# Performance work log

Measured on AMD Instinct MI355X. Metric: run time of the kernel, lower is better.

Reference implementation:

```python
import jax, jax.numpy as jnp
import numpy as np

K, N = 64, 4096

def setup_inputs() -> dict:
    key = jax.random.key(0)
    k1, k2 = jax.random.split(key)
    zs = jax.random.uniform(k1, (K, N), dtype=jnp.float32)        # K candidate schedules
    X = jax.random.uniform(k2, (N, N), dtype=jnp.float32)         # channel gain matrix
    var_noise = jnp.asarray(1.0, dtype=jnp.float32)
    return {"zs": zs, "X": X, "var_noise": var_noise}

def reference(zs, X, var_noise):
    # Original per-sample math: all_info[i,j] = z[j]*X[i,j]
    #   numerators   = diag(all_info) = z * diag(X)
    #   denominators = row_sum(all_info) - numerators = X @ z - numerators
    # Batched over K zs: one GEMM instead of K O(n^2) elementwise products.
    row_sums = jnp.einsum('kn,in->ki', zs, X)       # [K, N] = (X @ z_k)_i
    numerators = zs * jnp.diagonal(X)[None, :]      # [K, N]
    denominators = row_sums - numerators            # [K, N]
    per_sample = -jnp.sum(numerators / (var_noise + denominators), axis=1)  # [K]
    return jnp.sum(per_sample) / zs.shape[0]
```

## Files before the change

### kernel.cpp

```cpp
#include <hip/hip_runtime.h>

#define N_DIM 4096

typedef float f4  __attribute__((ext_vector_type(4)));
typedef short s8v __attribute__((ext_vector_type(8)));

#if defined(__has_builtin)
#if __has_builtin(__builtin_amdgcn_cvt_pk_bf16_f32)
#define HAVE_CVT_PK 1
#endif
#endif

static __device__ __forceinline__ unsigned int f2bf_pair(float lo, float hi) {
#ifdef HAVE_CVT_PK
    typedef __bf16 bf2 __attribute__((ext_vector_type(2)));
    bf2 p = __builtin_amdgcn_cvt_pk_bf16_f32(lo, hi);
    return __builtin_bit_cast(unsigned int, p);
#else
    unsigned int ul = __builtin_bit_cast(unsigned int, lo);
    unsigned int uh = __builtin_bit_cast(unsigned int, hi);
    ul = ul + 0x7fffu + ((ul >> 16) & 1u);
    uh = uh + 0x7fffu + ((uh >> 16) & 1u);
    return (uh & 0xffff0000u) | (ul >> 16);
#endif
}

static __device__ __forceinline__ s8v cvt8(f4 a, f4 b) {
    unsigned int u4[4] = { f2bf_pair(a[0], a[1]), f2bf_pair(a[2], a[3]),
                           f2bf_pair(b[0], b[1]), f2bf_pair(b[2], b[3]) };
    return __builtin_bit_cast(s8v, u4);
}

#define MFMA(a, b, c) __builtin_amdgcn_mfma_f32_16x16x32_bf16((a), (b), (c), 0, 0, 0)

__global__ void zero_out_kernel(float* __restrict__ out) {
    if (threadIdx.x == 0 && blockIdx.x == 0) out[0] = 0.f;
}

__global__ __launch_bounds__(256) void gemm_part_kernel(
    const float* __restrict__ zs, const float* __restrict__ X,
    float* __restrict__ part) {
    __shared__ s8v zsP[2][512];
    __shared__ s8v xP [2][512];

    const int tid  = threadIdx.x;
    const int lane = tid & 63;
    const int w    = tid >> 6;
    const int n0   = blockIdx.x * 512;
    const int i0   = blockIdx.y * 64;

    const int r0  = tid >> 3;
    const int cid = (tid & 7) * 8;
    const int stp = (tid >> 2) & 1;
    const int csb = tid & 3;
    const int g0  = (((r0 >> 4) * 2 + stp) << 6) | (r0 & 15) | (csb << 4);
    const int g1  = ((((r0 + 32) >> 4) * 2 + stp) << 6) | (r0 & 15) | (csb << 4);

    const float* gz0 = zs + (size_t)r0 * N_DIM + n0 + cid;
    const float* gz1 = zs + (size_t)(r0 + 32) * N_DIM + n0 + cid;
    const float* gx0 = X  + (size_t)(i0 + r0) * N_DIM + n0 + cid;
    const float* gx1 = X  + (size_t)(i0 + r0 + 32) * N_DIM + n0 + cid;

    f4 rz[4], rx[4];
    rz[0] = *(const f4*)(gz0);     rz[1] = *(const f4*)(gz0 + 4);
    rz[2] = *(const f4*)(gz1);     rz[3] = *(const f4*)(gz1 + 4);
    rx[0] = *(const f4*)(gx0);     rx[1] = *(const f4*)(gx0 + 4);
    rx[2] = *(const f4*)(gx1);     rx[3] = *(const f4*)(gx1 + 4);

    f4 acc[2][2] = {};
    const int kh = (w & 1) * 2;
    const int ih = (w >> 1) * 2;

    for (int c = 0; c < 8; ++c) {
        const int buf = c & 1;
        s8v pz0 = cvt8(rz[0], rz[1]);
        s8v pz1 = cvt8(rz[2], rz[3]);
        s8v px0 = cvt8(rx[0], rx[1]);
        s8v px1 = cvt8(rx[2], rx[3]);
        if (c < 7) {
            const int off = (c + 1) * 64;
            rz[0] = *(const f4*)(gz0 + off); rz[1] = *(const f4*)(gz0 + off + 4);
            rz[2] = *(const f4*)(gz1 + off); rz[3] = *(const f4*)(gz1 + off + 4);
            rx[0] = *(const f4*)(gx0 + off); rx[1] = *(const f4*)(gx0 + off + 4);
            rx[2] = *(const f4*)(gx1 + off); rx[3] = *(const f4*)(gx1 + off + 4);
        }
        zsP[buf][g0] = pz0;  zsP[buf][g1] = pz1;
        xP[buf][g0]  = px0;  xP[buf][g1]  = px1;
        asm volatile("s_waitcnt lgkmcnt(0)\n\ts_barrier" ::: "memory");

        s8v a0s0 = zsP[buf][((kh    ) * 2 + 0) * 64 + lane];
        s8v a0s1 = zsP[buf][((kh    ) * 2 + 1) * 64 + lane];
        s8v a1s0 = zsP[buf][((kh + 1) * 2 + 0) * 64 + lane];
        s8v a1s1 = zsP[buf][((kh + 1) * 2 + 1) * 64 + lane];
        s8v b0s0 = xP [buf][((ih    ) * 2 + 0) * 64 + lane];
        s8v b0s1 = xP [buf][((ih    ) * 2 + 1) * 64 + lane];
        s8v b1s0 = xP [buf][((ih + 1) * 2 + 0) * 64 + lane];
        s8v b1s1 = xP [buf][((ih + 1) * 2 + 1) * 64 + lane];

        acc[0][0] = MFMA(a0s0, b0s0, acc[0][0]);
        acc[0][1] = MFMA(a0s0, b1s0, acc[0][1]);
        acc[1][0] = MFMA(a1s0, b0s0, acc[1][0]);
        acc[1][1] = MFMA(a1s0, b1s0, acc[1][1]);
        acc[0][0] = MFMA(a0s1, b0s1, acc[0][0]);
        acc[0][1] = MFMA(a0s1, b1s1, acc[0][1]);
        acc[1][0] = MFMA(a1s1, b0s1, acc[1][0]);
        acc[1][1] = MFMA(a1s1, b1s1, acc[1][1]);
    }

    f4* pp = (f4*)part;
    const int base = (blockIdx.x * 64 + blockIdx.y) * 4;
    #pragma unroll
    for (int a = 0; a < 2; ++a)
        #pragma unroll
        for (int b = 0; b < 2; ++b)
            pp[((base + kh + a) * 4 + ih + b) * 64 + lane] = acc[a][b];
}

__global__ __launch_bounds__(256) void epilogue_kernel(
    const float* __restrict__ part, const float* __restrict__ zs,
    const float* __restrict__ X, const float* __restrict__ varp,
    float* __restrict__ out) {
    const int tid = threadIdx.x;
    const int idx = blockIdx.x * 256 + tid;
    const int k = idx >> 12, i = idx & (N_DIM - 1);
    const int it = i >> 6, itl = (i >> 4) & 3, kt = k >> 4;
    const int lane = ((k & 12) << 2) | (i & 15);
    const int r    = k & 3;

    float s = 0.f;
    #pragma unroll
    for (int ne = 0; ne < 8; ++ne)
        s += part[((((ne * 64 + it) * 4 + kt) * 4 + itl) * 64 + lane) * 4 + r];

    const float num = zs[(size_t)k * N_DIM + i] * X[(size_t)i * (N_DIM + 1)];
    const float den = s - num;
    float v = num / (varp[0] + den);

    #pragma unroll
    for (int off = 32; off >= 1; off >>= 1) v += __shfl_down(v, off);
    __shared__ float wsum[4];
    if ((tid & 63) == 0) wsum[tid >> 6] = v;
    __syncthreads();
    if (tid == 0)
        atomicAdd(out, -(wsum[0] + wsum[1] + wsum[2] + wsum[3]) * (1.0f / 64.0f));
}

extern "C" void kernel_launch(void* const* d_in, const int* in_sizes, int n_in,
                              void* d_out, int out_size, void* d_ws, size_t ws_size,
                              hipStream_t stream) {
    const float* zs   = (const float*)d_in[0];
    const float* X    = (const float*)d_in[1];
    const float* varp = (const float*)d_in[2];
    float* out  = (float*)d_out;
    float* part = (float*)d_ws;

    hipLaunchKernelGGL(zero_out_kernel, dim3(1), dim3(64), 0, stream, out);
    hipLaunchKernelGGL(gemm_part_kernel, dim3(8, 64), dim3(256), 0, stream, zs, X, part);
    hipLaunchKernelGGL(epilogue_kernel, dim3((64 * N_DIM) / 256), dim3(256), 0, stream,
                       part, zs, X, varp, out);
}
```

Baseline: 117.2 us.

## Fuse epilogue into GEMM via last-block-done counter and double split-K

Merges the separate epilogue kernel into the GEMM kernel. Each row-tile keeps an atomic counter, and the last of its split-K blocks reduces the partials and computes the SINR terms. The split-K factor also goes from 8 to 16, halving the K range each block covers, so the grid has more blocks to fill the GPU. This removes a kernel launch and the extra global traffic of a separate pass, at the cost of atomics, thread fences, and a serialized tail reduction inside one block per tile.

```diff
diff --git a/kernel.cpp b/kernel.cpp
--- a/kernel.cpp
+++ b/kernel.cpp
@@ -1,6 +1,7 @@
 #include <hip/hip_runtime.h>
 
 #define N_DIM 4096
+#define NE    16
 
 typedef float f4  __attribute__((ext_vector_type(4)));
 typedef short s8v __attribute__((ext_vector_type(8)));
@@ -33,20 +34,22 @@
 
 #define MFMA(a, b, c) __builtin_amdgcn_mfma_f32_16x16x32_bf16((a), (b), (c), 0, 0, 0)
 
-__global__ void zero_out_kernel(float* __restrict__ out) {
-    if (threadIdx.x == 0 && blockIdx.x == 0) out[0] = 0.f;
+__global__ void zero_kernel(float* __restrict__ out, int* __restrict__ cnt) {
+    if (threadIdx.x < 64) cnt[threadIdx.x] = 0;
+    if (threadIdx.x == 0) out[0] = 0.f;
 }
 
-__global__ __launch_bounds__(256) void gemm_part_kernel(
+__global__ __launch_bounds__(256) void gemm_fused_kernel(
     const float* __restrict__ zs, const float* __restrict__ X,
-    float* __restrict__ part) {
+    const float* __restrict__ varp, float* __restrict__ part,
+    int* __restrict__ cnt, float* __restrict__ out) {
     __shared__ s8v zsP[2][512];
     __shared__ s8v xP [2][512];
 
     const int tid  = threadIdx.x;
     const int lane = tid & 63;
     const int w    = tid >> 6;
-    const int n0   = blockIdx.x * 512;
+    const int n0   = blockIdx.x * 256;
     const int i0   = blockIdx.y * 64;
 
     const int r0  = tid >> 3;
@@ -71,13 +74,13 @@
     const int kh = (w & 1) * 2;
     const int ih = (w >> 1) * 2;
 
-    for (int c = 0; c < 8; ++c) {
+    for (int c = 0; c < 4; ++c) {
         const int buf = c & 1;
         s8v pz0 = cvt8(rz[0], rz[1]);
         s8v pz1 = cvt8(rz[2], rz[3]);
         s8v px0 = cvt8(rx[0], rx[1]);
         s8v px1 = cvt8(rx[2], rx[3]);
-        if (c < 7) {
+        if (c < 3) {
             const int off = (c + 1) * 64;
             rz[0] = *(const f4*)(gz0 + off); rz[1] = *(const f4*)(gz0 + off + 4);
             rz[2] = *(const f4*)(gz1 + off); rz[3] = *(const f4*)(gz1 + off + 4);
@@ -108,38 +111,50 @@
     }
 
     f4* pp = (f4*)part;
-    const int base = (blockIdx.x * 64 + blockIdx.y) * 4;
+    const int tb = (blockIdx.y * NE + blockIdx.x) * 1024;
     #pragma unroll
     for (int a = 0; a < 2; ++a)
         #pragma unroll
         for (int b = 0; b < 2; ++b)
-            pp[((base + kh + a) * 4 + ih + b) * 64 + lane] = acc[a][b];
-}
+            pp[tb + ((kh + a) * 4 + (ih + b)) * 64 + lane] = acc[a][b];
 
-__global__ __launch_bounds__(256) void epilogue_kernel(
-    const float* __restrict__ part, const float* __restrict__ zs,
-    const float* __restrict__ X, const float* __restrict__ varp,
-    float* __restrict__ out) {
-    const int tid = threadIdx.x;
-    const int idx = blockIdx.x * 256 + tid;
-    const int k = idx >> 12, i = idx & (N_DIM - 1);
-    const int it = i >> 6, itl = (i >> 4) & 3, kt = k >> 4;
-    const int lane = ((k & 12) << 2) | (i & 15);
-    const int r    = k & 3;
+    __threadfence();
+    __shared__ int lastf;
+    if (tid == 0) lastf = (atomicAdd(&cnt[blockIdx.y], 1) == NE - 1);
+    __syncthreads();
+    if (!lastf) return;
+    __threadfence();
 
-    float s = 0.f;
+    f4 s[4] = {};
+    for (int ne = 0; ne < NE; ++ne) {
+        const f4* q = pp + (blockIdx.y * NE + ne) * 1024 + tid * 4;
+        #pragma unroll
+        for (int jj = 0; jj < 4; ++jj) s[jj] += q[jj];
+    }
+    const int j0  = tid * 4;
+    const int kt  = j0 >> 8;
+    const int itl = (j0 >> 6) & 3;
+    const int ln0 = j0 & 63;
+    const int k0  = kt * 16 + (ln0 >> 4) * 4;
+    const int ib  = blockIdx.y * 64 + itl * 16 + (ln0 & 15);
+    const float var = varp[0];
+
+    float vsum = 0.f;
     #pragma unroll
-    for (int ne = 0; ne < 8; ++ne)
-        s += part[((((ne * 64 + it) * 4 + kt) * 4 + itl) * 64 + lane) * 4 + r];
-
-    const float num = zs[(size_t)k * N_DIM + i] * X[(size_t)i * (N_DIM + 1)];
-    const float den = s - num;
-    float v = num / (varp[0] + den);
-
+    for (int c2 = 0; c2 < 4; ++c2) {
+        const int   i  = ib + c2;
+        const float dg = X[(size_t)i * (N_DIM + 1)];
+        #pragma unroll
+        for (int r = 0; r < 4; ++r) {
+            float num = zs[(size_t)(k0 + r) * N_DIM + i] * dg;
+            float den = s[c2][r] - num;
+            vsum += num / (var + den);
+        }
+    }
     #pragma unroll
-    for (int off = 32; off >= 1; off >>= 1) v += __shfl_down(v, off);
+    for (int off = 32; off >= 1; off >>= 1) vsum += __shfl_down(vsum, off);
     __shared__ float wsum[4];
-    if ((tid & 63) == 0) wsum[tid >> 6] = v;
+    if (lane == 0) wsum[w] = vsum;
     __syncthreads();
     if (tid == 0)
         atomicAdd(out, -(wsum[0] + wsum[1] + wsum[2] + wsum[3]) * (1.0f / 64.0f));
@@ -153,9 +168,9 @@
     const float* varp = (const float*)d_in[2];
     float* out  = (float*)d_out;
     float* part = (float*)d_ws;
+    int*   cnt  = (int*)((char*)d_ws + (size_t)64 * NE * 1024 * 16);
 
-    hipLaunchKernelGGL(zero_out_kernel, dim3(1), dim3(64), 0, stream, out);
-    hipLaunchKernelGGL(gemm_part_kernel, dim3(8, 64), dim3(256), 0, stream, zs, X, part);
-    hipLaunchKernelGGL(epilogue_kernel, dim3((64 * N_DIM) / 256), dim3(256), 0, stream,
-                       part, zs, X, varp, out);
+    hipLaunchKernelGGL(zero_kernel, dim3(1), dim3(64), 0, stream, out, cnt);
+    hipLaunchKernelGGL(gemm_fused_kernel, dim3(NE, 64), dim3(256), 0, stream,
+                       zs, X, varp, part, cnt, out);
 }
```

After: 263.3 us. 125% more time.
